# Kernel tuning notes

Hardware: AMD Instinct MI355X
Metric: run time of the kernel (lower is better)

Reference implementation:

```python
import jax, jax.numpy as jnp
import numpy as np

T_IN, B, D, H, L = 513, 128, 1024, 1024, 2


def setup_inputs() -> dict:
    key = jax.random.key(0)
    ks = jax.random.split(key, 12)
    s = 1.0 / np.sqrt(H)  # torch RNN init scale (uniform bound); use scaled normal
    return {
        "X": jax.random.normal(ks[0], (T_IN, B, D), jnp.float32),
        "Y": jax.random.normal(ks[1], (T_IN - 1, B, D), jnp.float32),
        "enc_Wih": jax.random.normal(ks[2], (L, H, D), jnp.float32) * s,
        "enc_Whh": jax.random.normal(ks[3], (L, H, H), jnp.float32) * s,
        "enc_bih": jax.random.normal(ks[4], (L, H), jnp.float32) * s,
        "enc_bhh": jax.random.normal(ks[5], (L, H), jnp.float32) * s,
        "dec_Wih": jax.random.normal(ks[6], (L, H, D), jnp.float32) * s,
        "dec_Whh": jax.random.normal(ks[7], (L, H, H), jnp.float32) * s,
        "dec_bih": jax.random.normal(ks[8], (L, H), jnp.float32) * s,
        "dec_bhh": jax.random.normal(ks[9], (L, H), jnp.float32) * s,
        "lin_W": jax.random.normal(ks[10], (D, H), jnp.float32) * s,
        "lin_b": jax.random.normal(ks[11], (D,), jnp.float32) * s,
    }


def _stack_step(h, x, Wih, Whh, bih, bhh):
    """One Elman step through L stacked layers. h: [L,B,H], x: [B,D] -> (h', top)."""
    n_layers = Wih.shape[0]
    new_h = []
    inp = x
    for l in range(n_layers):
        hl = jnp.tanh(inp @ Wih[l].T + bih[l] + h[l] @ Whh[l].T + bhh[l])
        new_h.append(hl)
        inp = hl
    return jnp.stack(new_h), inp


def reference(X, Y, enc_Wih, enc_Whh, enc_bih, enc_bhh,
              dec_Wih, dec_Whh, dec_bih, dec_bhh, lin_W, lin_b):
    t_in, batch = X.shape[0], X.shape[1]
    hidden = enc_Whh.shape[-1]
    n_layers = enc_Whh.shape[0]
    h0 = jnp.zeros((n_layers, batch, hidden), X.dtype)

    # Encoder: nn.RNN over X[:-1]
    def enc_step(h, x):
        h2, _ = _stack_step(h, x, enc_Wih, enc_Whh, enc_bih, enc_bhh)
        return h2, None
    hT, _ = jax.lax.scan(enc_step, h0, X[:-1])

    # Decoder (training / teacher forcing): inputs are [X[-1], Y[0], ..., Y[T_out-2]]
    t_out = t_in - 1
    dec_in = jnp.concatenate([X[-1:], Y[: t_out - 1]], axis=0)  # [T_out, B, D]

    def dec_step(h, x):
        h2, top = _stack_step(h, x, dec_Wih, dec_Whh, dec_bih, dec_bhh)
        return h2, top
    _, tops = jax.lax.scan(dec_step, hT, dec_in)  # [T_out, B, H]

    logits = tops @ lin_W.T + lin_b  # [T_out, B, out_dim]
    return jax.nn.log_softmax(logits, axis=-1)
```

## Files before the change

### kernel.cpp

```cpp
#include <hip/hip_runtime.h>


typedef _Float16 f16;
typedef _Float16 f16x8 __attribute__((ext_vector_type(8)));
typedef _Float16 f16x4 __attribute__((ext_vector_type(4)));
typedef float    f32x4 __attribute__((ext_vector_type(4)));
typedef unsigned long long u64;

#define MFMA16(a, b, c) __builtin_amdgcn_mfma_f32_16x16x32_f16((a), (b), (c), 0, 0, 0)

__device__ __forceinline__ f32x4 zero4() {
  f32x4 v; v[0] = 0.f; v[1] = 0.f; v[2] = 0.f; v[3] = 0.f; return v;
}

__device__ __forceinline__ f16x8 cvt8(const float* __restrict__ p) {
  float4 a = *(const float4*)p;
  float4 b = *(const float4*)(p + 4);
  f16x8 r;
  r[0] = (f16)a.x; r[1] = (f16)a.y; r[2] = (f16)a.z; r[3] = (f16)a.w;
  r[4] = (f16)b.x; r[5] = (f16)b.y; r[6] = (f16)b.z; r[7] = (f16)b.w;
  return r;
}

__device__ __forceinline__ float fast_tanh(float x) {
  float e = __expf(2.f * x);
  return 1.f - 2.f / (e + 1.f);
}

__device__ __forceinline__ void st8_ag(f16* p, f16x4 v) {
  asm volatile("global_store_dwordx2 %0, %1, off sc1" :: "v"(p), "v"(v) : "memory");
}
__device__ __forceinline__ f16x4 ld8_sync(const f16* p) {
  f16x4 r;
  asm volatile("global_load_dwordx2 %0, %1, off sc0\n\ts_waitcnt vmcnt(0)"
               : "=&v"(r) : "v"(p) : "memory");
  return r;
}

#define WLOAD8(dst, base)                                                     \
  asm volatile(                                                               \
      "global_load_dwordx4 %0, %8, off\n\t"                                   \
      "global_load_dwordx4 %1, %8, off offset:64\n\t"                         \
      "global_load_dwordx4 %2, %8, off offset:128\n\t"                        \
      "global_load_dwordx4 %3, %8, off offset:192\n\t"                        \
      "global_load_dwordx4 %4, %8, off offset:256\n\t"                        \
      "global_load_dwordx4 %5, %8, off offset:320\n\t"                        \
      "global_load_dwordx4 %6, %8, off offset:384\n\t"                        \
      "global_load_dwordx4 %7, %8, off offset:448\n\t"                        \
      "s_waitcnt vmcnt(0)"                                                    \
      : "=&v"(dst[0]), "=&v"(dst[1]), "=&v"(dst[2]), "=&v"(dst[3]),           \
        "=&v"(dst[4]), "=&v"(dst[5]), "=&v"(dst[6]), "=&v"(dst[7])            \
      : "v"(base) : "memory")

template <typename AT, bool BF16, bool OUT_F16>
__global__ __launch_bounds__(256)
void gemm_bias(const AT* __restrict__ A1, const AT* __restrict__ A2, int rowSplit,
               const void* __restrict__ B, const float* __restrict__ bias1,
               const float* __restrict__ bias2, void* __restrict__ outp,
               int M, int N, int K)
{
  __shared__ f16 Ash[128 * 64];
  __shared__ f16 Bsh[128 * 64];
  const int t = threadIdx.x;
  const int w = t >> 6, l = t & 63;
  const int wm = w >> 1, wn = w & 1;
  const int lrow = l & 15, lk8 = (l >> 4) * 8;
  const int m0 = blockIdx.y * 128, n0 = blockIdx.x * 128;
  const int sr = t >> 3;
  const int skf = (t & 7) * 8;

  f32x4 acc[4][4];
#pragma unroll
  for (int i = 0; i < 4; ++i)
#pragma unroll
    for (int j = 0; j < 4; ++j) acc[i][j] = zero4();

  f16x8 ar[4], br[4];

  auto loadA = [&](int r, int k) -> f16x8 {
    const int row = m0 + r;
    if constexpr (sizeof(AT) == 4) {
      const float* src = (row < rowSplit) ? ((const float*)A1 + (size_t)row * K)
                                          : ((const float*)A2 + (size_t)(row - rowSplit) * K);
      return cvt8(src + k);
    } else {
      const f16* src = (row < rowSplit) ? ((const f16*)A1 + (size_t)row * K)
                                        : ((const f16*)A2 + (size_t)(row - rowSplit) * K);
      return *(const f16x8*)(src + k);
    }
  };
  auto loadB = [&](int r, int k) -> f16x8 {
    if constexpr (BF16) return *(const f16x8*)((const f16*)B + (size_t)(n0 + r) * K + k);
    else                return cvt8((const float*)B + (size_t)(n0 + r) * K + k);
  };

#pragma unroll
  for (int s = 0; s < 4; ++s) { ar[s] = loadA(s * 32 + sr, skf); br[s] = loadB(s * 32 + sr, skf); }

  const int nkt = K >> 6;
  for (int kt = 0; kt < nkt; ++kt) {
#pragma unroll
    for (int s = 0; s < 4; ++s) {
      const int r = s * 32 + sr;
      const int di = r * 64 + (skf ^ ((r & 7) << 3));
      *(f16x8*)(Ash + di) = ar[s];
      *(f16x8*)(Bsh + di) = br[s];
    }
    __syncthreads();
    if (kt + 1 < nkt) {
      const int k0 = (kt + 1) << 6;
#pragma unroll
      for (int s = 0; s < 4; ++s) { ar[s] = loadA(s * 32 + sr, k0 + skf); br[s] = loadB(s * 32 + sr, k0 + skf); }
    }
#pragma unroll
    for (int ks = 0; ks < 2; ++ks) {
      const int kb = ks * 32 + lk8;
      f16x8 af[4], bf[4];
#pragma unroll
      for (int mt = 0; mt < 4; ++mt) {
        const int r = wm * 64 + mt * 16 + lrow;
        af[mt] = *(const f16x8*)(Ash + r * 64 + (kb ^ ((r & 7) << 3)));
      }
#pragma unroll
      for (int nt = 0; nt < 4; ++nt) {
        const int r = wn * 64 + nt * 16 + lrow;
        bf[nt] = *(const f16x8*)(Bsh + r * 64 + (kb ^ ((r & 7) << 3)));
      }
#pragma unroll
      for (int mt = 0; mt < 4; ++mt)
#pragma unroll
        for (int nt = 0; nt < 4; ++nt)
          acc[mt][nt] = MFMA16(af[mt], bf[nt], acc[mt][nt]);
    }
    __syncthreads();
  }

#pragma unroll
  for (int nt = 0; nt < 4; ++nt) {
    const int col = n0 + wn * 64 + nt * 16 + lrow;
    const float bv = bias1[col] + (bias2 ? bias2[col] : 0.f);
#pragma unroll
    for (int mt = 0; mt < 4; ++mt) {
#pragma unroll
      for (int r = 0; r < 4; ++r) {
        const int row = m0 + wm * 64 + mt * 16 + (l >> 4) * 4 + r;
        const float v = acc[mt][nt][r] + bv;
        if constexpr (OUT_F16) ((f16*)outp)[(size_t)row * N + col] = (f16)v;
        else                   ((float*)outp)[(size_t)row * N + col] = v;
      }
    }
  }
}

__global__ __launch_bounds__(256)
void cvt_w3(const float* __restrict__ s0, const float* __restrict__ s1,
            const float* __restrict__ s2, f16* __restrict__ dst)
{
  const float* s = (blockIdx.y == 0) ? s0 : (blockIdx.y == 1) ? s1 : s2;
  const size_t base = (size_t)blockIdx.y << 20;
  const int i = (blockIdx.x * 256 + threadIdx.x) * 4;
  float4 v = *(const float4*)(s + i);
  f16x4 o;
  o[0] = (f16)v.x; o[1] = (f16)v.y; o[2] = (f16)v.z; o[3] = (f16)v.w;
  *(f16x4*)(dst + base + i) = o;
}

__global__ __launch_bounds__(256)
void cvt_w1(const float* __restrict__ s, f16* __restrict__ dst)
{
  const int i = (blockIdx.x * 256 + threadIdx.x) * 4;
  float4 v = *(const float4*)(s + i);
  f16x4 o;
  o[0] = (f16)v.x; o[1] = (f16)v.y; o[2] = (f16)v.z; o[3] = (f16)v.w;
  *(f16x4*)(dst + i) = o;
}

__global__ __launch_bounds__(256, 1)
void rnn_phase(const f16* __restrict__ pre0,
               f16* __restrict__ h0b,
               f16* __restrict__ h1b,
               unsigned* flags,
               const f16* __restrict__ W0f, const f16* __restrict__ W1f,
               const f16* __restrict__ W2f,
               const float* __restrict__ bih1, const float* __restrict__ bhh1,
               f16* __restrict__ tops,
               int s_base)
{
  __shared__ float pbuf[8][16][36];

  const int t = threadIdx.x;
  const int w = t >> 6, l = t & 63;
  const int lrow = l & 15, lk8 = (l >> 4) * 8;
  const int bid = blockIdx.x;
  const int g = bid & 7, slice = bid >> 3;
  const int rbase = g * 16, c0 = slice * 32;
  const bool is_dec = (s_base != 0);
  const int kw = w * 256;

  f16x8 wv0[2][8], wv1[2][8], wv2[2][8];
#pragma unroll
  for (int ct = 0; ct < 2; ++ct) {
    const size_t wr = (size_t)(c0 + ct * 16 + lrow) * 1024 + kw + lk8;
    WLOAD8(wv0[ct], W0f + wr);
    WLOAD8(wv1[ct], W1f + wr);
    WLOAD8(wv2[ct], W2f + wr);
  }
  __builtin_amdgcn_sched_barrier(0);

  const int ep_p = t >> 7;
  const int sub = t & 127;
  const int ep_r = sub >> 3;
  const int ep_c = (sub & 7) * 4;
  float b1v[4];
#pragma unroll
  for (int i = 0; i < 4; ++i)
    b1v[i] = bih1[c0 + ep_c + i] + bhh1[c0 + ep_c + i];

  const int fidx = (g << 5) + slice;
  const f16* prep_base = pre0 + ((size_t)(rbase + ep_r)) * 1024 + c0 + ep_c;

  unsigned* octet_fp = flags + (g << 5) + (w << 3) + (l & 7);

  f16x4 pre_next;
#pragma unroll
  for (int i = 0; i < 4; ++i) pre_next[i] = (f16)0.f;
  if (ep_p == 0)
    pre_next = *(const f16x4*)prep_base;

  for (int s_loc = 0; s_loc <= 512; ++s_loc) {
    const int s = s_base + s_loc;
    const f16x4 pre4 = pre_next;

    if ((s_loc & 7) == 0) {
      if (t == 0)
        asm volatile("buffer_inv\n\ts_waitcnt vmcnt(0)" ::: "memory");
      __syncthreads();
    }

    if (s_loc > 0) {
      const unsigned tgt = (unsigned)s_loc;
      int it = 0;
      for (;;) {
        unsigned v;
        if (((++it) & 7) == 0) {
          v = __hip_atomic_load(octet_fp, __ATOMIC_RELAXED, __HIP_MEMORY_SCOPE_AGENT);
          if (__all((l < 8) ? (int)(v >= tgt) : 1)) break;
          __builtin_amdgcn_s_sleep(1);
        } else {
          asm volatile("global_load_dword %0, %1, off sc0\n\ts_waitcnt vmcnt(0)"
                       : "=&v"(v) : "v"(octet_fp) : "memory");
          if (__all((l < 8) ? (int)(v >= tgt) : 1)) break;
        }
      }
    }

    const int R0 = (s + 15) & 15, Wr0 = s & 15;
    const int R1 = (s + 14) & 15, Wr1 = (s + 15) & 15;
    const f16* h0p = h0b + (size_t)R0 * 131072;
    const f16* h1p = h1b + (size_t)R1 * 131072;
    f16* h0w = h0b + (size_t)Wr0 * 131072;
    f16* h1w = h1b + (size_t)Wr1 * 131072;
    const bool cmp_h0 = (s_loc < 512);
    const bool h1_copy = (is_dec && s_loc == 0);
    const bool cmp_h1 = !((!is_dec && s_loc == 0) || h1_copy);

    f16x8 A[8], C[8];
    const f16* ap = h0p + (size_t)(rbase + lrow) * 1024 + kw + lk8;
    const f16* cp = h1p + (size_t)(rbase + lrow) * 1024 + kw + lk8;
    asm volatile(
        "global_load_dwordx4 %0, %16, off sc0\n\t"
        "global_load_dwordx4 %1, %16, off offset:64 sc0\n\t"
        "global_load_dwordx4 %2, %16, off offset:128 sc0\n\t"
        "global_load_dwordx4 %3, %16, off offset:192 sc0\n\t"
        "global_load_dwordx4 %4, %16, off offset:256 sc0\n\t"
        "global_load_dwordx4 %5, %16, off offset:320 sc0\n\t"
        "global_load_dwordx4 %6, %16, off offset:384 sc0\n\t"
        "global_load_dwordx4 %7, %16, off offset:448 sc0\n\t"
        "global_load_dwordx4 %8, %17, off sc0\n\t"
        "global_load_dwordx4 %9, %17, off offset:64 sc0\n\t"
        "global_load_dwordx4 %10, %17, off offset:128 sc0\n\t"
        "global_load_dwordx4 %11, %17, off offset:192 sc0\n\t"
        "global_load_dwordx4 %12, %17, off offset:256 sc0\n\t"
        "global_load_dwordx4 %13, %17, off offset:320 sc0\n\t"
        "global_load_dwordx4 %14, %17, off offset:384 sc0\n\t"
        "global_load_dwordx4 %15, %17, off offset:448 sc0\n\t"
        "s_waitcnt vmcnt(0)"
        : "=&v"(A[0]), "=&v"(A[1]), "=&v"(A[2]), "=&v"(A[3]),
          "=&v"(A[4]), "=&v"(A[5]), "=&v"(A[6]), "=&v"(A[7]),
          "=&v"(C[0]), "=&v"(C[1]), "=&v"(C[2]), "=&v"(C[3]),
          "=&v"(C[4]), "=&v"(C[5]), "=&v"(C[6]), "=&v"(C[7])
        : "v"(ap), "v"(cp)
        : "memory");
    __builtin_amdgcn_sched_barrier(0);

    f32x4 acc0[2], acc1[2];
    acc0[0] = zero4(); acc0[1] = zero4(); acc1[0] = zero4(); acc1[1] = zero4();

#pragma unroll
    for (int j = 0; j < 8; ++j) {
#pragma unroll
      for (int ct = 0; ct < 2; ++ct) {
        acc0[ct] = MFMA16(A[j], wv0[ct][j], acc0[ct]);
        acc1[ct] = MFMA16(A[j], wv1[ct][j], acc1[ct]);
        acc1[ct] = MFMA16(C[j], wv2[ct][j], acc1[ct]);
      }
    }

#pragma unroll
    for (int ct = 0; ct < 2; ++ct)
#pragma unroll
      for (int r = 0; r < 4; ++r) {
        const int row = (l >> 4) * 4 + r;
        pbuf[w * 2 + 0][row][ct * 16 + lrow] = acc0[ct][r];
        pbuf[w * 2 + 1][row][ct * 16 + lrow] = acc1[ct][r];
      }
    __syncthreads();

    if (ep_p == 0) {
      if (cmp_h0) {
        f32x4 sa = zero4();
#pragma unroll
        for (int ww = 0; ww < 4; ++ww)
          sa += *(const f32x4*)&pbuf[ww * 2 + 0][ep_r][ep_c];
        f16x4 o;
#pragma unroll
        for (int i = 0; i < 4; ++i) o[i] = (f16)fast_tanh(sa[i] + (float)pre4[i]);
        st8_ag(h0w + (size_t)(rbase + ep_r) * 1024 + c0 + ep_c, o);
      } else {
        f16x4 v = ld8_sync(h0p + (size_t)(rbase + ep_r) * 1024 + c0 + ep_c);
        st8_ag(h0w + (size_t)(rbase + ep_r) * 1024 + c0 + ep_c, v);
      }
    } else {
      if (cmp_h1) {
        f32x4 sa = zero4();
#pragma unroll
        for (int ww = 0; ww < 4; ++ww)
          sa += *(const f32x4*)&pbuf[ww * 2 + 1][ep_r][ep_c];
        f16x4 o;
#pragma unroll
        for (int i = 0; i < 4; ++i) o[i] = (f16)fast_tanh(sa[i] + b1v[i]);
        st8_ag(h1w + (size_t)(rbase + ep_r) * 1024 + c0 + ep_c, o);
        if (tops && s_loc >= 1)
          *(f16x4*)(tops + ((size_t)(s_loc - 1) * 128 + rbase + ep_r) * 1024 + c0 + ep_c) = o;
      } else if (h1_copy) {
        f16x4 v = ld8_sync(h1p + (size_t)(rbase + ep_r) * 1024 + c0 + ep_c);
        st8_ag(h1w + (size_t)(rbase + ep_r) * 1024 + c0 + ep_c, v);
      }
    }
    asm volatile("s_waitcnt vmcnt(0)" ::: "memory");
    __syncthreads();

    if (s_loc == 512) break;

    if (t == 0) {
      const unsigned val = (unsigned)(s_loc + 1);
      asm volatile("global_store_dword %0, %1, off sc0 sc1"
                   :: "v"(flags + fidx), "v"(val) : "memory");
    }
    if (ep_p == 0 && s_loc < 511)
      pre_next = *(const f16x4*)(prep_base + (size_t)(s_loc + 1) * 131072);
  }
}

__global__ __launch_bounds__(256)
void logsoftmax_rows(float* __restrict__ x)
{
  const int row = blockIdx.x;
  const int t = threadIdx.x;
  float* p = x + (size_t)row * 1024;
  float4 v = ((float4*)p)[t];
  float m = fmaxf(fmaxf(v.x, v.y), fmaxf(v.z, v.w));
#pragma unroll
  for (int off = 32; off >= 1; off >>= 1) m = fmaxf(m, __shfl_xor(m, off));
  __shared__ float red[4];
  __shared__ float red2[4];
  const int w = t >> 6;
  if ((t & 63) == 0) red[w] = m;
  __syncthreads();
  m = fmaxf(fmaxf(red[0], red[1]), fmaxf(red[2], red[3]));
  float s = __expf(v.x - m) + __expf(v.y - m) + __expf(v.z - m) + __expf(v.w - m);
#pragma unroll
  for (int off = 32; off >= 1; off >>= 1) s += __shfl_xor(s, off);
  if ((t & 63) == 0) red2[w] = s;
  __syncthreads();
  s = red2[0] + red2[1] + red2[2] + red2[3];
  const float lse = m + __logf(s);
  v.x -= lse; v.y -= lse; v.z -= lse; v.w -= lse;
  ((float4*)p)[t] = v;
}

extern "C" void kernel_launch(void* const* d_in, const int* in_sizes, int n_in,
                              void* d_out, int out_size, void* d_ws, size_t ws_size,
                              hipStream_t stream)
{
  (void)in_sizes; (void)n_in; (void)out_size; (void)ws_size;

  const float* X    = (const float*)d_in[0];
  const float* Y    = (const float*)d_in[1];
  const float* eWih = (const float*)d_in[2];
  const float* eWhh = (const float*)d_in[3];
  const float* ebih = (const float*)d_in[4];
  const float* ebhh = (const float*)d_in[5];
  const float* dWih = (const float*)d_in[6];
  const float* dWhh = (const float*)d_in[7];
  const float* dbih = (const float*)d_in[8];
  const float* dbhh = (const float*)d_in[9];
  const float* linW = (const float*)d_in[10];
  const float* linb = (const float*)d_in[11];

  char* ws = (char*)d_ws;
  unsigned* flags = (unsigned*)ws;
  f16* h0b  = (f16*)(ws + 65536);
  f16* h1b  = (f16*)(ws + 65536 + (16u << 18));
  f16* wcvt = (f16*)(ws + (9u << 20));
  f16* pre0 = (f16*)(ws + (16u << 20));
  f16* tops = (f16*)(ws + (144u << 20));
  f16* tmpB = tops;

  const size_t LAYER1 = 1024 * 1024;
  const size_t MEG = 1024 * 1024;
  const int M = 512 * 128;

  hipMemsetAsync(d_ws, 0, 65536 + (32u << 18), stream);

  dim3 ggrid(8, 512);
  dim3 cgrid3(1024, 3);

  cvt_w1<<<1024, 256, 0, stream>>>(eWih, tmpB);
  gemm_bias<float, true, true><<<ggrid, 256, 0, stream>>>(
      X, X, 1 << 30, tmpB, ebih, ebhh, pre0, M, 1024, 1024);

  cvt_w3<<<cgrid3, 256, 0, stream>>>(eWhh, eWih + LAYER1, eWhh + LAYER1, wcvt);
  rnn_phase<<<256, 256, 0, stream>>>(
      pre0, h0b, h1b, flags,
      wcvt, wcvt + MEG, wcvt + 2 * MEG, ebih + 1024, ebhh + 1024,
      nullptr, 0);

  cvt_w1<<<1024, 256, 0, stream>>>(dWih, tmpB);
  gemm_bias<float, true, true><<<ggrid, 256, 0, stream>>>(
      X + (size_t)512 * 128 * 1024, Y, 128, tmpB, dbih, dbhh, pre0, M, 1024, 1024);

  hipMemsetAsync(d_ws, 0, 4096, stream);

  cvt_w3<<<cgrid3, 256, 0, stream>>>(dWhh, dWih + LAYER1, dWhh + LAYER1, wcvt);
  rnn_phase<<<256, 256, 0, stream>>>(
      pre0, h0b, h1b, flags,
      wcvt, wcvt + MEG, wcvt + 2 * MEG, dbih + 1024, dbhh + 1024,
      tops, 513);

  cvt_w1<<<1024, 256, 0, stream>>>(linW, wcvt);
  gemm_bias<f16, true, false><<<ggrid, 256, 0, stream>>>(
      tops, tops, 1 << 30, wcvt, linb, nullptr, d_out, M, 1024, 1024);

  logsoftmax_rows<<<M, 256, 0, stream>>>((float*)d_out);
}
```

Measured before the change: 5.058 ms.

## Split per-layer readiness flags so layer-0 and layer-1 work overlap across blocks

Replaces the single per-step flag array with separate flag sets for layer-0 and layer-1 hidden states. Each block waits only on the layer-0 flags before loading h0 and running its MFMAs, then waits on the layer-1 flags before loading h1. Within a block, LDS counters let one wave signal each layer's epilogue completion, so those flags are published early instead of after a full block barrier. This aims to shorten the critical path of the grid-wide recurrence, at the cost of more complex spin-wait ordering and a new risk of deadlock or memory-ordering bugs.

```diff
diff --git a/kernel.cpp b/kernel.cpp
--- a/kernel.cpp
+++ b/kernel.cpp
@@ -179,7 +179,7 @@
 void rnn_phase(const f16* __restrict__ pre0,
                f16* __restrict__ h0b,
                f16* __restrict__ h1b,
-               unsigned* flags,
+               unsigned* sync,
                const f16* __restrict__ W0f, const f16* __restrict__ W1f,
                const f16* __restrict__ W2f,
                const float* __restrict__ bih1, const float* __restrict__ bhh1,
@@ -187,6 +187,7 @@
                int s_base)
 {
   __shared__ float pbuf[8][16][36];
+  __shared__ unsigned hs0, hs1;
 
   const int t = threadIdx.x;
   const int w = t >> 6, l = t & 63;
@@ -197,6 +198,11 @@
   const bool is_dec = (s_base != 0);
   const int kw = w * 256;
 
+  unsigned* flags0 = sync;
+  unsigned* flags1 = sync + 256;
+
+  if (t == 0) { hs0 = 0; hs1 = 0; }
+
   f16x8 wv0[2][8], wv1[2][8], wv2[2][8];
 #pragma unroll
   for (int ct = 0; ct < 2; ++ct) {
@@ -219,7 +225,9 @@
   const int fidx = (g << 5) + slice;
   const f16* prep_base = pre0 + ((size_t)(rbase + ep_r)) * 1024 + c0 + ep_c;
 
-  unsigned* octet_fp = flags + (g << 5) + (w << 3) + (l & 7);
+  const int octoff = (g << 5) + (w << 3) + (l & 7);
+  unsigned* oct0 = flags0 + octoff;
+  unsigned* oct1 = flags1 + octoff;
 
   f16x4 pre_next;
 #pragma unroll
@@ -235,23 +243,6 @@
       if (t == 0)
         asm volatile("buffer_inv\n\ts_waitcnt vmcnt(0)" ::: "memory");
       __syncthreads();
-    }
-
-    if (s_loc > 0) {
-      const unsigned tgt = (unsigned)s_loc;
-      int it = 0;
-      for (;;) {
-        unsigned v;
-        if (((++it) & 7) == 0) {
-          v = __hip_atomic_load(octet_fp, __ATOMIC_RELAXED, __HIP_MEMORY_SCOPE_AGENT);
-          if (__all((l < 8) ? (int)(v >= tgt) : 1)) break;
-          __builtin_amdgcn_s_sleep(1);
-        } else {
-          asm volatile("global_load_dword %0, %1, off sc0\n\ts_waitcnt vmcnt(0)"
-                       : "=&v"(v) : "v"(octet_fp) : "memory");
-          if (__all((l < 8) ? (int)(v >= tgt) : 1)) break;
-        }
-      }
     }
 
     const int R0 = (s + 15) & 15, Wr0 = s & 15;
@@ -264,33 +255,26 @@
     const bool h1_copy = (is_dec && s_loc == 0);
     const bool cmp_h1 = !((!is_dec && s_loc == 0) || h1_copy);
 
-    f16x8 A[8], C[8];
+    if (s_loc > 0) {
+      const unsigned tgt = (unsigned)s_loc;
+      int it = 0;
+      for (;;) {
+        unsigned v;
+        if (((++it) & 7) == 0) {
+          v = __hip_atomic_load(oct0, __ATOMIC_RELAXED, __HIP_MEMORY_SCOPE_AGENT);
+          if (__all((l < 8) ? (int)(v >= tgt) : 1)) break;
+          __builtin_amdgcn_s_sleep(1);
+        } else {
+          asm volatile("global_load_dword %0, %1, off sc0\n\ts_waitcnt vmcnt(0)"
+                       : "=&v"(v) : "v"(oct0) : "memory");
+          if (__all((l < 8) ? (int)(v >= tgt) : 1)) break;
+        }
+      }
+    }
+
+    f16x8 A[8];
     const f16* ap = h0p + (size_t)(rbase + lrow) * 1024 + kw + lk8;
-    const f16* cp = h1p + (size_t)(rbase + lrow) * 1024 + kw + lk8;
-    asm volatile(
-        "global_load_dwordx4 %0, %16, off sc0\n\t"
-        "global_load_dwordx4 %1, %16, off offset:64 sc0\n\t"
-        "global_load_dwordx4 %2, %16, off offset:128 sc0\n\t"
-        "global_load_dwordx4 %3, %16, off offset:192 sc0\n\t"
-        "global_load_dwordx4 %4, %16, off offset:256 sc0\n\t"
-        "global_load_dwordx4 %5, %16, off offset:320 sc0\n\t"
-        "global_load_dwordx4 %6, %16, off offset:384 sc0\n\t"
-        "global_load_dwordx4 %7, %16, off offset:448 sc0\n\t"
-        "global_load_dwordx4 %8, %17, off sc0\n\t"
-        "global_load_dwordx4 %9, %17, off offset:64 sc0\n\t"
-        "global_load_dwordx4 %10, %17, off offset:128 sc0\n\t"
-        "global_load_dwordx4 %11, %17, off offset:192 sc0\n\t"
-        "global_load_dwordx4 %12, %17, off offset:256 sc0\n\t"
-        "global_load_dwordx4 %13, %17, off offset:320 sc0\n\t"
-        "global_load_dwordx4 %14, %17, off offset:384 sc0\n\t"
-        "global_load_dwordx4 %15, %17, off offset:448 sc0\n\t"
-        "s_waitcnt vmcnt(0)"
-        : "=&v"(A[0]), "=&v"(A[1]), "=&v"(A[2]), "=&v"(A[3]),
-          "=&v"(A[4]), "=&v"(A[5]), "=&v"(A[6]), "=&v"(A[7]),
-          "=&v"(C[0]), "=&v"(C[1]), "=&v"(C[2]), "=&v"(C[3]),
-          "=&v"(C[4]), "=&v"(C[5]), "=&v"(C[6]), "=&v"(C[7])
-        : "v"(ap), "v"(cp)
-        : "memory");
+    WLOAD8(A, ap);
     __builtin_amdgcn_sched_barrier(0);
 
     f32x4 acc0[2], acc1[2];
@@ -302,8 +286,35 @@
       for (int ct = 0; ct < 2; ++ct) {
         acc0[ct] = MFMA16(A[j], wv0[ct][j], acc0[ct]);
         acc1[ct] = MFMA16(A[j], wv1[ct][j], acc1[ct]);
+      }
+    }
+
+    if (s_loc > 0) {
+      const unsigned tgt = (unsigned)s_loc;
+      int it = 0;
+      for (;;) {
+        unsigned v;
+        if (((++it) & 7) == 0) {
+          v = __hip_atomic_load(oct1, __ATOMIC_RELAXED, __HIP_MEMORY_SCOPE_AGENT);
+          if (__all((l < 8) ? (int)(v >= tgt) : 1)) break;
+          __builtin_amdgcn_s_sleep(1);
+        } else {
+          asm volatile("global_load_dword %0, %1, off sc0\n\ts_waitcnt vmcnt(0)"
+                       : "=&v"(v) : "v"(oct1) : "memory");
+          if (__all((l < 8) ? (int)(v >= tgt) : 1)) break;
+        }
+      }
+    }
+
+    f16x8 C[8];
+    const f16* cp = h1p + (size_t)(rbase + lrow) * 1024 + kw + lk8;
+    WLOAD8(C, cp);
+    __builtin_amdgcn_sched_barrier(0);
+#pragma unroll
+    for (int j = 0; j < 8; ++j) {
+#pragma unroll
+      for (int ct = 0; ct < 2; ++ct)
         acc1[ct] = MFMA16(C[j], wv2[ct][j], acc1[ct]);
-      }
     }
 
 #pragma unroll
@@ -330,6 +341,24 @@
         f16x4 v = ld8_sync(h0p + (size_t)(rbase + ep_r) * 1024 + c0 + ep_c);
         st8_ag(h0w + (size_t)(rbase + ep_r) * 1024 + c0 + ep_c, v);
       }
+      asm volatile("s_waitcnt vmcnt(0)" ::: "memory");
+      if (w == 1) {
+        if (l == 0)
+          __hip_atomic_store(&hs0, (unsigned)(s_loc + 1),
+                             __ATOMIC_RELEASE, __HIP_MEMORY_SCOPE_WORKGROUP);
+      } else {
+        if (l == 0) {
+          while (__hip_atomic_load(&hs0, __ATOMIC_ACQUIRE,
+                                   __HIP_MEMORY_SCOPE_WORKGROUP) < (unsigned)(s_loc + 1)) {}
+          if (s_loc < 512) {
+            const unsigned val = (unsigned)(s_loc + 1);
+            asm volatile("global_store_dword %0, %1, off sc0 sc1"
+                         :: "v"(flags0 + fidx), "v"(val) : "memory");
+          }
+        }
+      }
+      if (s_loc < 511)
+        pre_next = *(const f16x4*)(prep_base + (size_t)(s_loc + 1) * 131072);
     } else {
       if (cmp_h1) {
         f32x4 sa = zero4();
@@ -340,25 +369,36 @@
 #pragma unroll
         for (int i = 0; i < 4; ++i) o[i] = (f16)fast_tanh(sa[i] + b1v[i]);
         st8_ag(h1w + (size_t)(rbase + ep_r) * 1024 + c0 + ep_c, o);
-        if (tops && s_loc >= 1)
+        if (tops && s_loc >= 1) {
           *(f16x4*)(tops + ((size_t)(s_loc - 1) * 128 + rbase + ep_r) * 1024 + c0 + ep_c) = o;
+          asm volatile("s_waitcnt vmcnt(1)" ::: "memory");
+        } else {
+          asm volatile("s_waitcnt vmcnt(0)" ::: "memory");
+        }
       } else if (h1_copy) {
         f16x4 v = ld8_sync(h1p + (size_t)(rbase + ep_r) * 1024 + c0 + ep_c);
         st8_ag(h1w + (size_t)(rbase + ep_r) * 1024 + c0 + ep_c, v);
-      }
-    }
-    asm volatile("s_waitcnt vmcnt(0)" ::: "memory");
+        asm volatile("s_waitcnt vmcnt(0)" ::: "memory");
+      } else {
+        asm volatile("s_waitcnt vmcnt(0)" ::: "memory");
+      }
+      if (w == 3) {
+        if (l == 0)
+          __hip_atomic_store(&hs1, (unsigned)(s_loc + 1),
+                             __ATOMIC_RELEASE, __HIP_MEMORY_SCOPE_WORKGROUP);
+      } else {
+        if (l == 0) {
+          while (__hip_atomic_load(&hs1, __ATOMIC_ACQUIRE,
+                                   __HIP_MEMORY_SCOPE_WORKGROUP) < (unsigned)(s_loc + 1)) {}
+          if (s_loc < 512) {
+            const unsigned val = (unsigned)(s_loc + 1);
+            asm volatile("global_store_dword %0, %1, off sc0 sc1"
+                         :: "v"(flags1 + fidx), "v"(val) : "memory");
+          }
+        }
+      }
+    }
     __syncthreads();
-
-    if (s_loc == 512) break;
-
-    if (t == 0) {
-      const unsigned val = (unsigned)(s_loc + 1);
-      asm volatile("global_store_dword %0, %1, off sc0 sc1"
-                   :: "v"(flags + fidx), "v"(val) : "memory");
-    }
-    if (ep_p == 0 && s_loc < 511)
-      pre_next = *(const f16x4*)(prep_base + (size_t)(s_loc + 1) * 131072);
   }
 }
 
@@ -409,7 +449,7 @@
   const float* linb = (const float*)d_in[11];
 
   char* ws = (char*)d_ws;
-  unsigned* flags = (unsigned*)ws;
+  unsigned* sync = (unsigned*)ws;
   f16* h0b  = (f16*)(ws + 65536);
   f16* h1b  = (f16*)(ws + 65536 + (16u << 18));
   f16* wcvt = (f16*)(ws + (9u << 20));
@@ -432,7 +472,7 @@
 
   cvt_w3<<<cgrid3, 256, 0, stream>>>(eWhh, eWih + LAYER1, eWhh + LAYER1, wcvt);
   rnn_phase<<<256, 256, 0, stream>>>(
-      pre0, h0b, h1b, flags,
+      pre0, h0b, h1b, sync,
       wcvt, wcvt + MEG, wcvt + 2 * MEG, ebih + 1024, ebhh + 1024,
       nullptr, 0);
 
@@ -444,7 +484,7 @@
 
   cvt_w3<<<cgrid3, 256, 0, stream>>>(dWhh, dWih + LAYER1, dWhh + LAYER1, wcvt);
   rnn_phase<<<256, 256, 0, stream>>>(
-      pre0, h0b, h1b, flags,
+      pre0, h0b, h1b, sync,
       wcvt, wcvt + MEG, wcvt + 2 * MEG, dbih + 1024, dbhh + 1024,
       tops, 513);
 
```

Measured after the change: 5.388 ms. 1.07x slower.
